# Optimization experiments

Hardware: AMD Instinct MI355X
Metric: run time of the kernel (lower is better)

Reference implementation:

```python
import jax, jax.numpy as jnp
import numpy as np

N_ITEMS = 500000
EMBED_DIM = 64
BATCH = 1024


def setup_inputs() -> dict:
    key = jax.random.key(0)
    k_emb, k_idx = jax.random.split(key)
    item_embeddings = jax.random.normal(k_emb, (N_ITEMS, EMBED_DIM), dtype=jnp.float32)
    # 1-based indices in the original API; idx-1 in [-1, N-2] wraps identically in torch/jax
    item_idx = jax.random.randint(k_idx, (BATCH,), 0, N_ITEMS, dtype=jnp.int64)
    # Approximate the module's precomputed min/max sim scores with a 256-item sample
    sample = item_embeddings[:256]  # [256, d]
    sample_sim = sample @ item_embeddings.T  # [256, N]
    min_score = jnp.min(sample_sim).reshape(1)
    max_score = jnp.max(sample_sim).reshape(1)
    return {
        "item_embeddings": item_embeddings,
        "item_idx": item_idx,
        "min_score": min_score,
        "max_score": max_score,
    }


def reference(item_embeddings, item_idx, min_score, max_score):
    # item_embeddings: [N, d]; item_idx: [B] (1-based); min/max_score: [1]
    idx = item_idx - 1  # 0-based row into the table
    item_vector = item_embeddings[idx]  # [B, d]
    sim = item_vector @ item_embeddings.T  # [B, N]
    sim = (sim - min_score[0]) / (max_score[0] - min_score[0])
    # mask self-item
    batch = idx.shape[0]
    sim = sim.at[jnp.arange(batch), idx].set(-jnp.inf)
    # top-1
    scores = jnp.max(sim, axis=1)  # [B]
    indices = jnp.argmax(sim, axis=1) + 1  # back to 1-based, [B]
    return indices, scores
```

## Files before the change

kernel.cpp:

```cpp
#include <hip/hip_runtime.h>

#define N_ITEMS 500000
#define EMBED 64
#define BATCH 1024
#define NCH ((N_ITEMS + 127) / 128)
#define SEED_CH 512
#define CAP 4096
#define MARGIN 0.75f

typedef __attribute__((ext_vector_type(8))) __bf16 bf16x8;
typedef __attribute__((ext_vector_type(4))) float f32x4;

__device__ unsigned g_cand[BATCH * CAP];

__device__ __forceinline__ void cvt_hi(const f32x4 r0, const f32x4 r1, bf16x8& H) {
#pragma unroll
  for (int k = 0; k < 4; ++k) { H[k] = (__bf16)r0[k]; H[4 + k] = (__bf16)r1[k]; }
}

__device__ __forceinline__ float u2f(unsigned tu) {
  union { unsigned u; float f; } cv;
  cv.u = (tu & 0x80000000u) ? (tu & 0x7FFFFFFFu) : ~tu;
  return cv.f;
}

__device__ __forceinline__ float m3(float a, float b, float c) {
  return fmaxf(fmaxf(a, b), c);
}

template <int MODE>
__global__ __launch_bounds__(512, 4)
void scan_kernel(const float* __restrict__ emb, const int* __restrict__ idx,
                 unsigned* __restrict__ best_u, unsigned* __restrict__ cnt,
                 int climit, int stride) {
  __shared__ unsigned short Bb[2][128 * 64];
  __shared__ int sidx[512];

  const int tid = threadIdx.x, lane = tid & 63, wv = tid >> 6;
  const int l15 = lane & 15, kq = lane >> 4;
  const int bj = blockIdx.x, rh = blockIdx.y;
  const int m0 = wv * 64, rbase = rh * 512;

  {
    int row = idx[rbase + tid] - 1;
    if (row < 0) row += N_ITEMS;
    sidx[tid] = row;
  }
  const int sr = tid >> 2, sg = tid & 3;
  __syncthreads();

  bf16x8 ah[4][2];
#pragma unroll
  for (int am = 0; am < 4; ++am) {
    const float* src = emb + (size_t)sidx[m0 + am * 16 + l15] * EMBED + kq * 8;
    cvt_hi(*(const f32x4*)(src),      *(const f32x4*)(src + 4),  ah[am][0]);
    cvt_hi(*(const f32x4*)(src + 32), *(const f32x4*)(src + 36), ah[am][1]);
  }
  const int sw = sidx[m0 + lane];

  float bs[16];
  float Tm = 0.f;
#pragma unroll
  for (int am = 0; am < 4; ++am)
#pragma unroll
    for (int r = 0; r < 4; ++r) {
      const int sl = am * 4 + r;
      if (MODE == 0) {
        bs[sl] = -3.4e38f;
      } else {
        bs[sl] = u2f(best_u[rbase + m0 + am * 16 + kq * 4 + r]) - MARGIN;
      }
    }
  if (MODE == 1) {
    Tm = bs[0];
#pragma unroll
    for (int sl = 1; sl < 16; ++sl) Tm = fminf(Tm, bs[sl]);
  }

  f32x4 raw[4];
  {
    int jr = bj * 128 + sr;
    if (jr >= N_ITEMS) jr = N_ITEMS - 1;
    const float* s = emb + (size_t)jr * EMBED + sg * 16;
#pragma unroll
    for (int i = 0; i < 4; ++i) raw[i] = *(const f32x4*)(s + 4 * i);
  }

  int p = 0;
  for (int c = bj; c < climit; c += stride) {
    {
      bf16x8 H0, H1;
      cvt_hi(raw[0], raw[1], H0);
      cvt_hi(raw[2], raw[3], H1);
      const int g0 = (2 * sg) ^ (sr & 7), g1 = (2 * sg + 1) ^ (sr & 7);
      *(bf16x8*)(Bb[p] + sr * 64 + g0 * 8) = H0;
      *(bf16x8*)(Bb[p] + sr * 64 + g1 * 8) = H1;
    }
    __syncthreads();
    {
      int nc = c + stride;
      if (nc < climit) {
        int jr = nc * 128 + sr;
        if (jr >= N_ITEMS) jr = N_ITEMS - 1;
        const float* s = emb + (size_t)jr * EMBED + sg * 16;
#pragma unroll
        for (int i = 0; i < 4; ++i) raw[i] = *(const f32x4*)(s + 4 * i);
      }
    }

    const bool masked = (MODE == 0) && __any((sw >> 7) == c);

#pragma unroll
    for (int bn = 0; bn < 8; ++bn) {
      const int row16 = bn * 16 + l15;
      const int fro = row16 * 64;
      bf16x8 bh0 = *(const bf16x8*)(Bb[p] + fro + ((kq ^ (row16 & 7)) << 3));
      bf16x8 bh1 = *(const bf16x8*)(Bb[p] + fro + (((4 | kq) ^ (row16 & 7)) << 3));
      const f32x4 zero = {0.f, 0.f, 0.f, 0.f};
      f32x4 acc[4];
#pragma unroll
      for (int am = 0; am < 4; ++am) {
        acc[am] = __builtin_amdgcn_mfma_f32_16x16x32_bf16(ah[am][0], bh0, zero, 0, 0, 0);
        acc[am] = __builtin_amdgcn_mfma_f32_16x16x32_bf16(ah[am][1], bh1, acc[am], 0, 0, 0);
      }

      if (MODE == 0) {
        if (!masked) {
#pragma unroll
          for (int sl = 0; sl < 16; ++sl)
            bs[sl] = fmaxf(bs[sl], acc[sl >> 2][sl & 3]);
        } else {
          const int jc = c * 128 + bn * 16 + l15;
#pragma unroll
          for (int sl = 0; sl < 16; ++sl) {
            const int self = sidx[m0 + (sl >> 2) * 16 + kq * 4 + (sl & 3)];
            float v = (jc != self) ? acc[sl >> 2][sl & 3] : -3.4e38f;
            bs[sl] = fmaxf(bs[sl], v);
          }
        }
      } else {
        float t0 = m3(acc[0][0], acc[0][1], acc[0][2]);
        float t1 = m3(acc[0][3], acc[1][0], acc[1][1]);
        float t2 = m3(acc[1][2], acc[1][3], acc[2][0]);
        float t3 = m3(acc[2][1], acc[2][2], acc[2][3]);
        float t4 = m3(acc[3][0], acc[3][1], acc[3][2]);
        float gm = fmaxf(m3(t0, t1, t2), m3(t3, t4, acc[3][3]));
        if (__any(gm >= Tm)) {
          const int jc = c * 128 + bn * 16 + l15;
#pragma unroll
          for (int sl = 0; sl < 16; ++sl) {
            if (acc[sl >> 2][sl & 3] >= bs[sl] && jc < N_ITEMS) {
              const int gr = rbase + m0 + (sl >> 2) * 16 + kq * 4 + (sl & 3);
              unsigned pos = atomicAdd(cnt + gr, 1u);
              if (pos < CAP) g_cand[gr * CAP + pos] = (unsigned)jc;
            }
          }
        }
      }
    }
    p ^= 1;
  }

  if (MODE == 0) {
#pragma unroll
    for (int off = 1; off < 16; off <<= 1)
#pragma unroll
      for (int sl = 0; sl < 16; ++sl)
        bs[sl] = fmaxf(bs[sl], __shfl_xor(bs[sl], off, 64));
    if (l15 == 0) {
#pragma unroll
      for (int sl = 0; sl < 16; ++sl) {
        union { float f; int i; unsigned u; } cv; cv.f = bs[sl];
        unsigned mu = (cv.i < 0) ? ~cv.u : (cv.u | 0x80000000u);
        atomicMax(best_u + rbase + m0 + (sl >> 2) * 16 + kq * 4 + (sl & 3), mu);
      }
    }
  }
}

__global__ __launch_bounds__(512)
void rescore_kernel(const float* __restrict__ emb, const int* __restrict__ idx,
                    const unsigned* __restrict__ cnt,
                    const float* __restrict__ mn, const float* __restrict__ mx,
                    float* __restrict__ out, unsigned* __restrict__ ov_cnt,
                    unsigned* __restrict__ ov_rows) {
  const int lane = threadIdx.x & 63, wv = threadIdx.x >> 6;
  const int row = blockIdx.x * 8 + wv;
  int self = idx[row] - 1;
  if (self < 0) self += N_ITEMS;
  const float* a = emb + (size_t)self * EMBED;
  float av[EMBED];
#pragma unroll
  for (int k = 0; k < EMBED; k += 4) *(f32x4*)(av + k) = *(const f32x4*)(a + k);

  unsigned n = cnt[row];
  if (n > CAP) {
    if (lane == 0) {
      unsigned pos = atomicAdd(ov_cnt, 1u);
      ov_rows[pos] = (unsigned)row;
    }
    n = CAP;
  }
  float bv = -3.4e38f;
  unsigned bj = 0xFFFFFFFFu;
  for (unsigned i = lane; i < n; i += 64) {
    unsigned j = g_cand[row * CAP + i];
    if ((int)j == self) continue;
    const float* b = emb + (size_t)j * EMBED;
    float d = 0.f;
#pragma unroll
    for (int k = 0; k < EMBED; ++k) d = fmaf(av[k], b[k], d);
    if (d > bv || (d == bv && j < bj)) { bv = d; bj = j; }
  }
#pragma unroll
  for (int off = 1; off < 64; off <<= 1) {
    float ov = __shfl_xor(bv, off, 64);
    unsigned oj = (unsigned)__shfl_xor((int)bj, off, 64);
    if (ov > bv || (ov == bv && oj < bj)) { bv = ov; bj = oj; }
  }
  if (lane == 0) {
    float lo = mn[0], hi = mx[0];
    out[row] = (float)(bj + 1);
    out[BATCH + row] = (bv - lo) / (hi - lo);
  }
}

__global__ __launch_bounds__(256)
void cleanup_scan(const float* __restrict__ emb, const int* __restrict__ idx,
                  const unsigned* __restrict__ ov_cnt,
                  const unsigned* __restrict__ ov_rows,
                  unsigned long long* __restrict__ best64) {
  unsigned nov = *ov_cnt;
  if (nov == 0) return;
  if (nov > BATCH) nov = BATCH;
  __shared__ float av[EMBED];
  const int tid = threadIdx.x, lane = tid & 63;
  for (unsigned oi = 0; oi < nov; ++oi) {
    const int row = (int)ov_rows[oi];
    int self = idx[row] - 1;
    if (self < 0) self += N_ITEMS;
    __syncthreads();
    if (tid < EMBED) av[tid] = emb[(size_t)self * EMBED + tid];
    __syncthreads();
    const int j = blockIdx.x * 256 + tid;
    unsigned long long key = 0ull;
    if (j < N_ITEMS && j != self) {
      const float* b = emb + (size_t)j * EMBED;
      float d = 0.f;
#pragma unroll
      for (int k = 0; k < EMBED; ++k) d = fmaf(av[k], b[k], d);
      union { float f; int i; unsigned u; } cv; cv.f = d;
      unsigned mu = (cv.i < 0) ? ~cv.u : (cv.u | 0x80000000u);
      key = ((unsigned long long)mu << 32) |
            (unsigned long long)(0xFFFFFFFFu - (unsigned)j);
    }
#pragma unroll
    for (int off = 1; off < 64; off <<= 1) {
      unsigned long long ok = __shfl_xor(key, off, 64);
      if (ok > key) key = ok;
    }
    if (lane == 0) atomicMax(best64 + row, key);
  }
}

__global__ void cleanup_write(const unsigned* __restrict__ cnt,
                              const unsigned long long* __restrict__ best64,
                              const float* __restrict__ mn,
                              const float* __restrict__ mx,
                              float* __restrict__ out) {
  int r = blockIdx.x * blockDim.x + threadIdx.x;
  if (r >= BATCH) return;
  if (cnt[r] <= CAP) return;
  unsigned long long k = best64[r];
  unsigned mu = (unsigned)(k >> 32);
  unsigned j  = 0xFFFFFFFFu - (unsigned)(k & 0xFFFFFFFFull);
  union { unsigned u; float f; } cv;
  cv.u = (mu & 0x80000000u) ? (mu & 0x7FFFFFFFu) : ~mu;
  float lo = mn[0], hi = mx[0];
  out[r] = (float)(j + 1);
  out[BATCH + r] = (cv.f - lo) / (hi - lo);
}

extern "C" void kernel_launch(void* const* d_in, const int* in_sizes, int n_in,
                              void* d_out, int out_size, void* d_ws, size_t ws_size,
                              hipStream_t stream) {
  const float* emb = (const float*)d_in[0];
  const int* idx   = (const int*)d_in[1];
  const float* mn  = (const float*)d_in[2];
  const float* mx  = (const float*)d_in[3];
  unsigned* ws     = (unsigned*)d_ws;
  unsigned* best_u = ws;
  unsigned* cnt    = ws + 1024;
  unsigned* ov_cnt = ws + 2048;
  unsigned* ov_rows= ws + 2052;
  unsigned long long* best64 = (unsigned long long*)(ws + 3076);

  hipMemsetAsync(d_ws, 0, 3076 * 4 + 1024 * 8, stream);

  scan_kernel<0><<<dim3(256, 2), dim3(512), 0, stream>>>(emb, idx, best_u, cnt,
                                                         SEED_CH, 256);
  scan_kernel<1><<<dim3(512, 2), dim3(512), 0, stream>>>(emb, idx, best_u, cnt,
                                                         NCH, 512);
  rescore_kernel<<<dim3(BATCH / 8), dim3(512), 0, stream>>>(
      emb, idx, cnt, mn, mx, (float*)d_out, ov_cnt, ov_rows);
  cleanup_scan<<<dim3(2048), dim3(256), 0, stream>>>(emb, idx, ov_cnt, ov_rows,
                                                     best64);
  cleanup_write<<<dim3(4), dim3(256), 0, stream>>>(cnt, best64, mn, mx,
                                                   (float*)d_out);
}
```

Baseline: 308.7 us.

## Pre-convert table to swizzled bf16 and stage chunks via global_load_lds

A new prep kernel converts the fp32 embedding table once per call into a pre-swizzled bf16 copy in a global buffer. The scan kernels then load each 128-row chunk straight into LDS with async global_load_lds, replacing per-chunk register loads, bf16 conversion and LDS stores, and double-buffer the next chunk while the current one is computed. The scan grids are halved. This halves bytes read by the two scans and removes conversion work from the hot loop, at the cost of an extra full-table read and write pass plus a large global scratch buffer. Fewer blocks may also lower occupancy.

Result: no change. 311.4 us (+0.9%).

```diff
diff --git a/kernel.cpp b/kernel.cpp
--- a/kernel.cpp
+++ b/kernel.cpp
@@ -12,6 +12,7 @@
 typedef __attribute__((ext_vector_type(4))) float f32x4;
 
 __device__ unsigned g_cand[BATCH * CAP];
+__device__ unsigned short g_ebf[(size_t)NCH * 1024 * 8];
 
 __device__ __forceinline__ void cvt_hi(const f32x4 r0, const f32x4 r1, bf16x8& H) {
 #pragma unroll
@@ -26,6 +27,34 @@
 
 __device__ __forceinline__ float m3(float a, float b, float c) {
   return fmaxf(fmaxf(a, b), c);
+}
+
+__device__ __forceinline__ void gll16(const void* g, void* l) {
+  __builtin_amdgcn_global_load_lds(
+      (const __attribute__((address_space(1))) unsigned*)g,
+      (__attribute__((address_space(3))) unsigned*)l, 16, 0, 0);
+}
+
+__device__ __forceinline__ void stage_chunk(const unsigned short* gbase,
+                                            unsigned short* lbase, int tid, int wv) {
+  gll16(gbase + (size_t)tid * 8,         lbase + (size_t)(wv * 64) * 8);
+  gll16(gbase + (size_t)(512 + tid) * 8, lbase + (size_t)(512 + wv * 64) * 8);
+}
+
+__global__ __launch_bounds__(256)
+void prep_kernel(const float* __restrict__ emb) {
+  const int t = blockIdx.x * 256 + threadIdx.x;
+  const int gl = t & 1023;
+  const int c  = t >> 10;
+  const int r  = gl >> 3;
+  const int j  = gl & 7;
+  const int k  = j ^ (r & 7);
+  long row = (long)c * 128 + r;
+  if (row >= N_ITEMS) row = N_ITEMS - 1;
+  const float* s = emb + row * EMBED + k * 8;
+  bf16x8 h;
+  cvt_hi(*(const f32x4*)s, *(const f32x4*)(s + 4), h);
+  *(bf16x8*)(g_ebf + (size_t)t * 8) = h;
 }
 
 template <int MODE>
@@ -46,7 +75,6 @@
     if (row < 0) row += N_ITEMS;
     sidx[tid] = row;
   }
-  const int sr = tid >> 2, sg = tid & 3;
   __syncthreads();
 
   bf16x8 ah[4][2];
@@ -77,35 +105,16 @@
     for (int sl = 1; sl < 16; ++sl) Tm = fminf(Tm, bs[sl]);
   }
 
-  f32x4 raw[4];
-  {
-    int jr = bj * 128 + sr;
-    if (jr >= N_ITEMS) jr = N_ITEMS - 1;
-    const float* s = emb + (size_t)jr * EMBED + sg * 16;
-#pragma unroll
-    for (int i = 0; i < 4; ++i) raw[i] = *(const f32x4*)(s + 4 * i);
-  }
+  stage_chunk(g_ebf + (size_t)bj * 8192, Bb[0], tid, wv);
 
   int p = 0;
   for (int c = bj; c < climit; c += stride) {
-    {
-      bf16x8 H0, H1;
-      cvt_hi(raw[0], raw[1], H0);
-      cvt_hi(raw[2], raw[3], H1);
-      const int g0 = (2 * sg) ^ (sr & 7), g1 = (2 * sg + 1) ^ (sr & 7);
-      *(bf16x8*)(Bb[p] + sr * 64 + g0 * 8) = H0;
-      *(bf16x8*)(Bb[p] + sr * 64 + g1 * 8) = H1;
-    }
-    __syncthreads();
+    asm volatile("s_waitcnt vmcnt(0)" ::: "memory");
+    __builtin_amdgcn_s_barrier();
     {
       int nc = c + stride;
-      if (nc < climit) {
-        int jr = nc * 128 + sr;
-        if (jr >= N_ITEMS) jr = N_ITEMS - 1;
-        const float* s = emb + (size_t)jr * EMBED + sg * 16;
-#pragma unroll
-        for (int i = 0; i < 4; ++i) raw[i] = *(const f32x4*)(s + 4 * i);
-      }
+      if (nc < climit)
+        stage_chunk(g_ebf + (size_t)nc * 8192, Bb[p ^ 1], tid, wv);
     }
 
     const bool masked = (MODE == 0) && __any((sw >> 7) == c);
@@ -297,10 +306,12 @@
 
   hipMemsetAsync(d_ws, 0, 3076 * 4 + 1024 * 8, stream);
 
-  scan_kernel<0><<<dim3(256, 2), dim3(512), 0, stream>>>(emb, idx, best_u, cnt,
-                                                         SEED_CH, 256);
-  scan_kernel<1><<<dim3(512, 2), dim3(512), 0, stream>>>(emb, idx, best_u, cnt,
-                                                         NCH, 512);
+  prep_kernel<<<dim3(NCH * 4), dim3(256), 0, stream>>>(emb);
+
+  scan_kernel<0><<<dim3(128, 2), dim3(512), 0, stream>>>(emb, idx, best_u, cnt,
+                                                         SEED_CH, 128);
+  scan_kernel<1><<<dim3(256, 2), dim3(512), 0, stream>>>(emb, idx, best_u, cnt,
+                                                         NCH, 256);
   rescore_kernel<<<dim3(BATCH / 8), dim3(512), 0, stream>>>(
       emb, idx, cnt, mn, mx, (float*)d_out, ov_cnt, ov_rows);
   cleanup_scan<<<dim3(2048), dim3(256), 0, stream>>>(emb, idx, ov_cnt, ov_rows,
```

## Fuse seed and filter scans into one kernel with running thresholds

Applied to the files above, without the earlier changes.

Merges the seeding pass and the candidate-filter pass into one kernel. Each block warms up on its first chunk, publishes per-row maxima through atomicMax, then scans its remaining chunks while tightening a per-lane running threshold, and rescans the first chunk at the end so that chunk is also filtered. The separate overflow cleanup kernels are removed; rows that overflow the candidate buffer are brute-forced by one wavefront inside rescore. This removes a kernel launch and a full second read of the table, but thresholds are only block-local after warm-up and may admit more candidates, and an overflow row now costs a serial full scan.

New measurement: 331.9 us. 7.5% more time.

```diff
diff --git a/kernel.cpp b/kernel.cpp
--- a/kernel.cpp
+++ b/kernel.cpp
@@ -4,7 +4,7 @@
 #define EMBED 64
 #define BATCH 1024
 #define NCH ((N_ITEMS + 127) / 128)
-#define SEED_CH 512
+#define CSTRIDE 256
 #define CAP 4096
 #define MARGIN 0.75f
 
@@ -24,15 +24,18 @@
   return cv.f;
 }
 
+__device__ __forceinline__ unsigned f2u(float f) {
+  union { float f; int i; unsigned u; } cv; cv.f = f;
+  return (cv.i < 0) ? ~cv.u : (cv.u | 0x80000000u);
+}
+
 __device__ __forceinline__ float m3(float a, float b, float c) {
   return fmaxf(fmaxf(a, b), c);
 }
 
-template <int MODE>
 __global__ __launch_bounds__(512, 4)
-void scan_kernel(const float* __restrict__ emb, const int* __restrict__ idx,
-                 unsigned* __restrict__ best_u, unsigned* __restrict__ cnt,
-                 int climit, int stride) {
+void fused_scan(const float* __restrict__ emb, const int* __restrict__ idx,
+                unsigned* __restrict__ best_u, unsigned* __restrict__ cnt) {
   __shared__ unsigned short Bb[2][128 * 64];
   __shared__ int sidx[512];
 
@@ -58,24 +61,12 @@
   }
   const int sw = sidx[m0 + lane];
 
-  float bs[16];
-  float Tm = 0.f;
-#pragma unroll
-  for (int am = 0; am < 4; ++am)
-#pragma unroll
-    for (int r = 0; r < 4; ++r) {
-      const int sl = am * 4 + r;
-      if (MODE == 0) {
-        bs[sl] = -3.4e38f;
-      } else {
-        bs[sl] = u2f(best_u[rbase + m0 + am * 16 + kq * 4 + r]) - MARGIN;
-      }
-    }
-  if (MODE == 1) {
-    Tm = bs[0];
-#pragma unroll
-    for (int sl = 1; sl < 16; ++sl) Tm = fminf(Tm, bs[sl]);
-  }
+  float rm[16];
+  float Tm = 3.4e38f;
+#pragma unroll
+  for (int sl = 0; sl < 16; ++sl) rm[sl] = -3.4e38f;
+
+  const int nc = (NCH - 1 - bj) / CSTRIDE + 1;
 
   f32x4 raw[4];
   {
@@ -87,7 +78,8 @@
   }
 
   int p = 0;
-  for (int c = bj; c < climit; c += stride) {
+  for (int it = 0; it <= nc; ++it) {
+    const int c = (it < nc) ? bj + it * CSTRIDE : bj;
     {
       bf16x8 H0, H1;
       cvt_hi(raw[0], raw[1], H0);
@@ -98,9 +90,9 @@
     }
     __syncthreads();
     {
-      int nc = c + stride;
-      if (nc < climit) {
-        int jr = nc * 128 + sr;
+      if (it < nc) {
+        const int ncn = (it + 1 < nc) ? bj + (it + 1) * CSTRIDE : bj;
+        int jr = ncn * 128 + sr;
         if (jr >= N_ITEMS) jr = N_ITEMS - 1;
         const float* s = emb + (size_t)jr * EMBED + sg * 16;
 #pragma unroll
@@ -108,7 +100,8 @@
       }
     }
 
-    const bool masked = (MODE == 0) && __any((sw >> 7) == c);
+    const bool warm = (it == 0);
+    const bool masked = warm && __any((sw >> 7) == c);
 
 #pragma unroll
     for (int bn = 0; bn < 8; ++bn) {
@@ -124,18 +117,18 @@
         acc[am] = __builtin_amdgcn_mfma_f32_16x16x32_bf16(ah[am][1], bh1, acc[am], 0, 0, 0);
       }
 
-      if (MODE == 0) {
+      if (warm) {
         if (!masked) {
 #pragma unroll
           for (int sl = 0; sl < 16; ++sl)
-            bs[sl] = fmaxf(bs[sl], acc[sl >> 2][sl & 3]);
+            rm[sl] = fmaxf(rm[sl], acc[sl >> 2][sl & 3]);
         } else {
           const int jc = c * 128 + bn * 16 + l15;
 #pragma unroll
           for (int sl = 0; sl < 16; ++sl) {
             const int self = sidx[m0 + (sl >> 2) * 16 + kq * 4 + (sl & 3)];
             float v = (jc != self) ? acc[sl >> 2][sl & 3] : -3.4e38f;
-            bs[sl] = fmaxf(bs[sl], v);
+            rm[sl] = fmaxf(rm[sl], v);
           }
         }
       } else {
@@ -149,32 +142,45 @@
           const int jc = c * 128 + bn * 16 + l15;
 #pragma unroll
           for (int sl = 0; sl < 16; ++sl) {
-            if (acc[sl >> 2][sl & 3] >= bs[sl] && jc < N_ITEMS) {
+            float a = acc[sl >> 2][sl & 3];
+            if (a >= rm[sl] - MARGIN && jc < N_ITEMS) {
               const int gr = rbase + m0 + (sl >> 2) * 16 + kq * 4 + (sl & 3);
               unsigned pos = atomicAdd(cnt + gr, 1u);
               if (pos < CAP) g_cand[gr * CAP + pos] = (unsigned)jc;
+              const int self = sidx[m0 + (sl >> 2) * 16 + kq * 4 + (sl & 3)];
+              if (jc != self) rm[sl] = fmaxf(rm[sl], a);
             }
           }
+          float t = rm[0];
+#pragma unroll
+          for (int sl = 1; sl < 16; ++sl) t = fminf(t, rm[sl]);
+          Tm = t - MARGIN;
         }
       }
     }
+
+    if (it <= 1) {
+#pragma unroll
+      for (int off = 1; off < 16; off <<= 1)
+#pragma unroll
+        for (int sl = 0; sl < 16; ++sl)
+          rm[sl] = fmaxf(rm[sl], __shfl_xor(rm[sl], off, 64));
+#pragma unroll
+      for (int sl = 0; sl < 16; ++sl) {
+        float v = rm[sl];
+        if (l15 == 0) {
+          unsigned old = atomicMax(
+              best_u + rbase + m0 + (sl >> 2) * 16 + kq * 4 + (sl & 3), f2u(v));
+          if (old) v = fmaxf(v, u2f(old));
+        }
+        rm[sl] = __shfl(v, lane & 48, 64);
+      }
+      Tm = rm[0];
+#pragma unroll
+      for (int sl = 1; sl < 16; ++sl) Tm = fminf(Tm, rm[sl]);
+      Tm -= MARGIN;
+    }
     p ^= 1;
-  }
-
-  if (MODE == 0) {
-#pragma unroll
-    for (int off = 1; off < 16; off <<= 1)
-#pragma unroll
-      for (int sl = 0; sl < 16; ++sl)
-        bs[sl] = fmaxf(bs[sl], __shfl_xor(bs[sl], off, 64));
-    if (l15 == 0) {
-#pragma unroll
-      for (int sl = 0; sl < 16; ++sl) {
-        union { float f; int i; unsigned u; } cv; cv.f = bs[sl];
-        unsigned mu = (cv.i < 0) ? ~cv.u : (cv.u | 0x80000000u);
-        atomicMax(best_u + rbase + m0 + (sl >> 2) * 16 + kq * 4 + (sl & 3), mu);
-      }
-    }
   }
 }
 
@@ -182,8 +188,7 @@
 void rescore_kernel(const float* __restrict__ emb, const int* __restrict__ idx,
                     const unsigned* __restrict__ cnt,
                     const float* __restrict__ mn, const float* __restrict__ mx,
-                    float* __restrict__ out, unsigned* __restrict__ ov_cnt,
-                    unsigned* __restrict__ ov_rows) {
+                    float* __restrict__ out) {
   const int lane = threadIdx.x & 63, wv = threadIdx.x >> 6;
   const int row = blockIdx.x * 8 + wv;
   int self = idx[row] - 1;
@@ -193,24 +198,28 @@
 #pragma unroll
   for (int k = 0; k < EMBED; k += 4) *(f32x4*)(av + k) = *(const f32x4*)(a + k);
 
-  unsigned n = cnt[row];
-  if (n > CAP) {
-    if (lane == 0) {
-      unsigned pos = atomicAdd(ov_cnt, 1u);
-      ov_rows[pos] = (unsigned)row;
-    }
-    n = CAP;
-  }
+  const unsigned n = cnt[row];
   float bv = -3.4e38f;
   unsigned bj = 0xFFFFFFFFu;
-  for (unsigned i = lane; i < n; i += 64) {
-    unsigned j = g_cand[row * CAP + i];
-    if ((int)j == self) continue;
-    const float* b = emb + (size_t)j * EMBED;
-    float d = 0.f;
-#pragma unroll
-    for (int k = 0; k < EMBED; ++k) d = fmaf(av[k], b[k], d);
-    if (d > bv || (d == bv && j < bj)) { bv = d; bj = j; }
+  if (n > CAP) {
+    for (unsigned j = lane; j < N_ITEMS; j += 64) {
+      if ((int)j == self) continue;
+      const float* b = emb + (size_t)j * EMBED;
+      float d = 0.f;
+#pragma unroll
+      for (int k = 0; k < EMBED; ++k) d = fmaf(av[k], b[k], d);
+      if (d > bv || (d == bv && j < bj)) { bv = d; bj = j; }
+    }
+  } else {
+    for (unsigned i = lane; i < n; i += 64) {
+      unsigned j = g_cand[row * CAP + i];
+      if ((int)j == self) continue;
+      const float* b = emb + (size_t)j * EMBED;
+      float d = 0.f;
+#pragma unroll
+      for (int k = 0; k < EMBED; ++k) d = fmaf(av[k], b[k], d);
+      if (d > bv || (d == bv && j < bj)) { bv = d; bj = j; }
+    }
   }
 #pragma unroll
   for (int off = 1; off < 64; off <<= 1) {
@@ -223,62 +232,6 @@
     out[row] = (float)(bj + 1);
     out[BATCH + row] = (bv - lo) / (hi - lo);
   }
-}
-
-__global__ __launch_bounds__(256)
-void cleanup_scan(const float* __restrict__ emb, const int* __restrict__ idx,
-                  const unsigned* __restrict__ ov_cnt,
-                  const unsigned* __restrict__ ov_rows,
-                  unsigned long long* __restrict__ best64) {
-  unsigned nov = *ov_cnt;
-  if (nov == 0) return;
-  if (nov > BATCH) nov = BATCH;
-  __shared__ float av[EMBED];
-  const int tid = threadIdx.x, lane = tid & 63;
-  for (unsigned oi = 0; oi < nov; ++oi) {
-    const int row = (int)ov_rows[oi];
-    int self = idx[row] - 1;
-    if (self < 0) self += N_ITEMS;
-    __syncthreads();
-    if (tid < EMBED) av[tid] = emb[(size_t)self * EMBED + tid];
-    __syncthreads();
-    const int j = blockIdx.x * 256 + tid;
-    unsigned long long key = 0ull;
-    if (j < N_ITEMS && j != self) {
-      const float* b = emb + (size_t)j * EMBED;
-      float d = 0.f;
-#pragma unroll
-      for (int k = 0; k < EMBED; ++k) d = fmaf(av[k], b[k], d);
-      union { float f; int i; unsigned u; } cv; cv.f = d;
-      unsigned mu = (cv.i < 0) ? ~cv.u : (cv.u | 0x80000000u);
-      key = ((unsigned long long)mu << 32) |
-            (unsigned long long)(0xFFFFFFFFu - (unsigned)j);
-    }
-#pragma unroll
-    for (int off = 1; off < 64; off <<= 1) {
-      unsigned long long ok = __shfl_xor(key, off, 64);
-      if (ok > key) key = ok;
-    }
-    if (lane == 0) atomicMax(best64 + row, key);
-  }
-}
-
-__global__ void cleanup_write(const unsigned* __restrict__ cnt,
-                              const unsigned long long* __restrict__ best64,
-                              const float* __restrict__ mn,
-                              const float* __restrict__ mx,
-                              float* __restrict__ out) {
-  int r = blockIdx.x * blockDim.x + threadIdx.x;
-  if (r >= BATCH) return;
-  if (cnt[r] <= CAP) return;
-  unsigned long long k = best64[r];
-  unsigned mu = (unsigned)(k >> 32);
-  unsigned j  = 0xFFFFFFFFu - (unsigned)(k & 0xFFFFFFFFull);
-  union { unsigned u; float f; } cv;
-  cv.u = (mu & 0x80000000u) ? (mu & 0x7FFFFFFFu) : ~mu;
-  float lo = mn[0], hi = mx[0];
-  out[r] = (float)(j + 1);
-  out[BATCH + r] = (cv.f - lo) / (hi - lo);
 }
 
 extern "C" void kernel_launch(void* const* d_in, const int* in_sizes, int n_in,
@@ -291,20 +244,10 @@
   unsigned* ws     = (unsigned*)d_ws;
   unsigned* best_u = ws;
   unsigned* cnt    = ws + 1024;
-  unsigned* ov_cnt = ws + 2048;
-  unsigned* ov_rows= ws + 2052;
-  unsigned long long* best64 = (unsigned long long*)(ws + 3076);
-
-  hipMemsetAsync(d_ws, 0, 3076 * 4 + 1024 * 8, stream);
-
-  scan_kernel<0><<<dim3(256, 2), dim3(512), 0, stream>>>(emb, idx, best_u, cnt,
-                                                         SEED_CH, 256);
-  scan_kernel<1><<<dim3(512, 2), dim3(512), 0, stream>>>(emb, idx, best_u, cnt,
-                                                         NCH, 512);
+
+  hipMemsetAsync(d_ws, 0, 2048 * 4, stream);
+
+  fused_scan<<<dim3(CSTRIDE, 2), dim3(512), 0, stream>>>(emb, idx, best_u, cnt);
   rescore_kernel<<<dim3(BATCH / 8), dim3(512), 0, stream>>>(
-      emb, idx, cnt, mn, mx, (float*)d_out, ov_cnt, ov_rows);
-  cleanup_scan<<<dim3(2048), dim3(256), 0, stream>>>(emb, idx, ov_cnt, ov_rows,
-                                                     best64);
-  cleanup_write<<<dim3(4), dim3(256), 0, stream>>>(cnt, best64, mn, mx,
-                                                   (float*)d_out);
-}
+      emb, idx, cnt, mn, mx, (float*)d_out);
+}
```
